# Kernel tuning notes

Hardware: AMD Instinct MI355X
Metric: run time of the kernel (lower is better)

## Reference

```python
import jax, jax.numpy as jnp
import numpy as np


def _ste_sign(x):
    # sign with straight-through (identity) gradient, matching gradient_override_map({'Sign': 'Identity'})
    return x + jax.lax.stop_gradient(jnp.sign(x) - x)


def _ternarize(W):
    # threshold = 0.7 * mean(|W|)
    t = 0.7 * jnp.mean(jnp.abs(W))
    # alpha = mean of |W| over entries with |W| strictly beyond threshold
    pos = jnp.where(W > t, W, jnp.zeros_like(W))
    neg = jnp.where(W < -t, W, jnp.zeros_like(W))
    a = jnp.abs(pos + neg)
    n = jnp.sum(jnp.where(a > 0, jnp.ones_like(a), jnp.zeros_like(a)))
    alpha = jnp.sum(a) / n
    # ternary weights in {-1, 0, +1}: sign(sign(W+t) + sign(W-t))
    Wq = _ste_sign(_ste_sign(W + t) + _ste_sign(W - t))
    return alpha * Wq


def setup_inputs() -> dict:
    key = jax.random.key(0)
    kx, kw = jax.random.split(key)
    x = jax.random.normal(kx, (32, 56, 56, 256), dtype=jnp.float32)      # NHWC
    W = jax.random.normal(kw, (3, 3, 256, 256), dtype=jnp.float32) * 0.02  # HWIO, stddev=0.02 init
    b = jnp.zeros((256,), dtype=jnp.float32)
    return {"x": x, "W": W, "b": b}


def reference(x, W, b):
    Wq = _ternarize(W)
    y = jax.lax.conv_general_dilated(
        x, Wq,
        window_strides=(1, 1),
        padding='SAME',
        dimension_numbers=('NHWC', 'HWIO', 'NHWC'),
    )
    return y + b  # act = identity
```

## Files before the change

kernel.cpp:

```cpp
#include <hip/hip_runtime.h>
#include <hip/hip_bf16.h>
#include <stdint.h>


typedef __attribute__((ext_vector_type(8))) short short8;
typedef __attribute__((ext_vector_type(4))) float floatx4;

#define Q40 1099511627776.0
#define INV_Q40 (1.0 / 1099511627776.0)
#define NW_ELEMS 589824
#define K_TOTAL 2304
#define WQT_OFF 512
#define XPAD_OFF 2360320
#define RED_BLOCKS 288

__device__ __forceinline__ void async16(const void* g, void* l) {
  __builtin_amdgcn_global_load_lds(
      (const __attribute__((address_space(1))) void*)g,
      (__attribute__((address_space(3))) void*)l, 16, 0, 0);
}

__device__ __forceinline__ ushort f2bf(float f) {
  __hip_bfloat16 h = __float2bfloat16(f);
  return *reinterpret_cast<ushort*>(&h);
}

__global__ __launch_bounds__(256) void pad_kernel(const float* __restrict__ x,
                                                  ushort* __restrict__ xpad) {
  uint idx = blockIdx.x * 256 + threadIdx.x;
  uint c8 = idx & 31;
  uint sp = idx >> 5;
  uint ww = sp % 58;
  uint t = sp / 58;
  uint hh = t % 58;
  uint n = t / 58;
  ushort* dst = xpad + ((size_t)sp * 256 + c8 * 8);
  if (hh == 0 || hh == 57 || ww == 0 || ww == 57) {
    uint4 z = {0, 0, 0, 0};
    *(uint4*)dst = z;
  } else {
    const float* src = x + (((size_t)(n * 56 + (hh - 1)) * 56 + (ww - 1)) * 256 + c8 * 8);
    float4 f0 = *(const float4*)src;
    float4 f1 = *(const float4*)(src + 4);
    ushort u[8];
    u[0] = f2bf(f0.x); u[1] = f2bf(f0.y); u[2] = f2bf(f0.z); u[3] = f2bf(f0.w);
    u[4] = f2bf(f1.x); u[5] = f2bf(f1.y); u[6] = f2bf(f1.z); u[7] = f2bf(f1.w);
    *(uint4*)dst = *(uint4*)u;
  }
}

__global__ __launch_bounds__(256) void sumabs_kernel(const float* __restrict__ W,
                                                     unsigned long long* __restrict__ scal) {
  __shared__ double sds[4];
  double v = 0.0;
#pragma unroll
  for (int j = 0; j < 8; j++) {
    uint i = (blockIdx.x * 8 + j) * 256 + threadIdx.x;
    v += (double)fabsf(W[i]);
  }
#pragma unroll
  for (int off = 32; off; off >>= 1) v += __shfl_down(v, off);
  if ((threadIdx.x & 63) == 0) sds[threadIdx.x >> 6] = v;
  __syncthreads();
  if (threadIdx.x == 0) {
    double s = sds[0] + sds[1] + sds[2] + sds[3];
    atomicAdd(&scal[0], (unsigned long long)(s * Q40 + 0.5));
  }
}

__global__ __launch_bounds__(256) void quant_kernel(const float* __restrict__ W,
                                                    ushort* __restrict__ WqT,
                                                    unsigned long long* __restrict__ scal) {
  __shared__ double sds[4];
  __shared__ unsigned long long cds[4];
  double s = (double)scal[0] * INV_Q40;
  float t = (float)(0.7 * (s / (double)NW_ELEMS));
  double v = 0.0;
  unsigned long long cnt = 0;
#pragma unroll
  for (int j = 0; j < 8; j++) {
    uint i = (blockIdx.x * 8 + j) * 256 + threadIdx.x;
    float w = W[i];
    bool pos = (w > t), neg = (w < -t);
    ushort q = pos ? (ushort)0x3F80 : (neg ? (ushort)0xBF80 : (ushort)0);
    uint k = i >> 8, co = i & 255;
    WqT[(size_t)co * K_TOTAL + k] = q;
    if (pos || neg) { v += (double)fabsf(w); cnt++; }
  }
#pragma unroll
  for (int off = 32; off; off >>= 1) {
    v += __shfl_down(v, off);
    cnt += __shfl_down(cnt, off);
  }
  if ((threadIdx.x & 63) == 0) { sds[threadIdx.x >> 6] = v; cds[threadIdx.x >> 6] = cnt; }
  __syncthreads();
  if (threadIdx.x == 0) {
    double sv = sds[0] + sds[1] + sds[2] + sds[3];
    unsigned long long sc = cds[0] + cds[1] + cds[2] + cds[3];
    atomicAdd(&scal[1], (unsigned long long)(sv * Q40 + 0.5));
    atomicAdd(&scal[2], sc);
  }
}

__global__ __launch_bounds__(256, 2) void conv_kernel(
    const ushort* __restrict__ xpad, const ushort* __restrict__ WqT,
    const unsigned long long* __restrict__ scal, const float* __restrict__ bias,
    float* __restrict__ out) {
  __shared__ __attribute__((aligned(16))) ushort Alds[128 * 64];
  __shared__ __attribute__((aligned(16))) ushort Blds[128 * 64];
  uint tid = threadIdx.x;
  uint bm = blockIdx.x >> 1, bn = blockIdx.x & 1;

  uint chunk = tid & 7;
  uint rbase = tid >> 3;
  const ushort* asrc[4];
  const ushort* bsrc[4];
#pragma unroll
  for (int i = 0; i < 4; i++) {
    uint row = i * 32 + rbase;
    uint gm = bm * 128 + row;
    uint n = gm / 3136;
    uint rem = gm - n * 3136;
    uint h = rem / 56;
    uint w = rem - h * 56;
    asrc[i] = xpad + (((size_t)(n * 58 + h) * 58 + w) * 256 + chunk * 8);
    bsrc[i] = WqT + ((size_t)(bn * 128 + row) * K_TOTAL + chunk * 8);
  }

  floatx4 acc[4][4];
#pragma unroll
  for (int mt = 0; mt < 4; mt++)
#pragma unroll
    for (int nt = 0; nt < 4; nt++) acc[mt][nt] = (floatx4){0.f, 0.f, 0.f, 0.f};

  uint lane = tid & 63;
  uint wv = tid >> 6;
  uint wm = wv >> 1, wn = wv & 1;
  uint fr = lane & 15, fq = lane >> 4;
  uint a_off = (wm * 64 + fr) * 128 + fq * 16;
  uint b_off = (wn * 64 + fr) * 128 + fq * 16;

  for (int ks = 0; ks < 36; ks++) {
    uint tap = (uint)ks >> 2;
    uint kc = ((uint)ks & 3) * 64;
    uint ky = tap / 3;
    uint kx = tap - ky * 3;
    uint aoffe = (ky * 58 + kx) * 256 + kc;
    uint boffe = (uint)ks * 64;

    __syncthreads();
#pragma unroll
    for (int i = 0; i < 4; i++)
      async16(asrc[i] + aoffe, (char*)Alds + i * 4096 + tid * 16);
#pragma unroll
    for (int i = 0; i < 4; i++)
      async16(bsrc[i] + boffe, (char*)Blds + i * 4096 + tid * 16);
    __syncthreads();

#pragma unroll
    for (int kk = 0; kk < 2; kk++) {
      short8 af[4], bfr[4];
#pragma unroll
      for (int mt = 0; mt < 4; mt++)
        af[mt] = *(const short8*)((const char*)Alds + a_off + mt * 2048 + kk * 64);
#pragma unroll
      for (int nt = 0; nt < 4; nt++)
        bfr[nt] = *(const short8*)((const char*)Blds + b_off + nt * 2048 + kk * 64);
#pragma unroll
      for (int mt = 0; mt < 4; mt++)
#pragma unroll
        for (int nt = 0; nt < 4; nt++)
          acc[mt][nt] = __builtin_amdgcn_mfma_f32_16x16x32_bf16(
              af[mt], bfr[nt], acc[mt][nt], 0, 0, 0);
    }
  }

  double sb = (double)scal[1] * INV_Q40;
  double cb = (double)scal[2];
  float alpha = (float)(sb / cb);
#pragma unroll
  for (int mt = 0; mt < 4; mt++) {
    uint mb = bm * 128 + wm * 64 + mt * 16 + fq * 4;
#pragma unroll
    for (int r = 0; r < 4; r++) {
      float* orow = out + (size_t)(mb + r) * 256;
#pragma unroll
      for (int nt = 0; nt < 4; nt++) {
        uint n = bn * 128 + wn * 64 + nt * 16 + fr;
        orow[n] = acc[mt][nt][r] * alpha + bias[n];
      }
    }
  }
}

extern "C" void kernel_launch(void* const* d_in, const int* in_sizes, int n_in,
                              void* d_out, int out_size, void* d_ws, size_t ws_size,
                              hipStream_t stream) {
  const float* x = (const float*)d_in[0];
  const float* W = (const float*)d_in[1];
  const float* b = (const float*)d_in[2];
  float* out = (float*)d_out;

  unsigned long long* scal = (unsigned long long*)d_ws;
  ushort* WqT = (ushort*)((char*)d_ws + WQT_OFF);
  ushort* xpad = (ushort*)((char*)d_ws + XPAD_OFF);

  hipMemsetAsync(d_ws, 0, 512, stream);

  pad_kernel<<<13454, 256, 0, stream>>>(x, xpad);
  sumabs_kernel<<<RED_BLOCKS, 256, 0, stream>>>(W, scal);
  quant_kernel<<<RED_BLOCKS, 256, 0, stream>>>(W, WqT, scal);
  conv_kernel<<<1568, 256, 0, stream>>>(xpad, WqT, scal, b, out);
}
```

Before: 349.4 us.

## Swizzle conv LDS tiles, reorder K loop by channel chunk, fuse pad with sumabs

```diff
diff --git a/kernel.cpp b/kernel.cpp
--- a/kernel.cpp
+++ b/kernel.cpp
@@ -13,6 +13,7 @@
 #define WQT_OFF 512
 #define XPAD_OFF 2360320
 #define RED_BLOCKS 288
+#define PAD_BLOCKS 13454
 
 __device__ __forceinline__ void async16(const void* g, void* l) {
   __builtin_amdgcn_global_load_lds(
@@ -25,9 +26,28 @@
   return *reinterpret_cast<ushort*>(&h);
 }
 
-__global__ __launch_bounds__(256) void pad_kernel(const float* __restrict__ x,
-                                                  ushort* __restrict__ xpad) {
-  uint idx = blockIdx.x * 256 + threadIdx.x;
+__global__ __launch_bounds__(256) void pad_sumabs_kernel(
+    const float* __restrict__ x, ushort* __restrict__ xpad,
+    const float* __restrict__ W, unsigned long long* __restrict__ scal) {
+  if (blockIdx.x < RED_BLOCKS) {
+    __shared__ double sds[4];
+    double v = 0.0;
+#pragma unroll
+    for (int j = 0; j < 8; j++) {
+      uint i = (blockIdx.x * 8 + j) * 256 + threadIdx.x;
+      v += (double)fabsf(W[i]);
+    }
+#pragma unroll
+    for (int off = 32; off; off >>= 1) v += __shfl_down(v, off);
+    if ((threadIdx.x & 63) == 0) sds[threadIdx.x >> 6] = v;
+    __syncthreads();
+    if (threadIdx.x == 0) {
+      double s = sds[0] + sds[1] + sds[2] + sds[3];
+      atomicAdd(&scal[0], (unsigned long long)(s * Q40 + 0.5));
+    }
+    return;
+  }
+  uint idx = (blockIdx.x - RED_BLOCKS) * 256 + threadIdx.x;
   uint c8 = idx & 31;
   uint sp = idx >> 5;
   uint ww = sp % 58;
@@ -49,25 +69,6 @@
   }
 }
 
-__global__ __launch_bounds__(256) void sumabs_kernel(const float* __restrict__ W,
-                                                     unsigned long long* __restrict__ scal) {
-  __shared__ double sds[4];
-  double v = 0.0;
-#pragma unroll
-  for (int j = 0; j < 8; j++) {
-    uint i = (blockIdx.x * 8 + j) * 256 + threadIdx.x;
-    v += (double)fabsf(W[i]);
-  }
-#pragma unroll
-  for (int off = 32; off; off >>= 1) v += __shfl_down(v, off);
-  if ((threadIdx.x & 63) == 0) sds[threadIdx.x >> 6] = v;
-  __syncthreads();
-  if (threadIdx.x == 0) {
-    double s = sds[0] + sds[1] + sds[2] + sds[3];
-    atomicAdd(&scal[0], (unsigned long long)(s * Q40 + 0.5));
-  }
-}
-
 __global__ __launch_bounds__(256) void quant_kernel(const float* __restrict__ W,
                                                     ushort* __restrict__ WqT,
                                                     unsigned long long* __restrict__ scal) {
@@ -113,6 +114,7 @@
 
   uint chunk = tid & 7;
   uint rbase = tid >> 3;
+  uint ceff = chunk ^ (rbase & 7);
   const ushort* asrc[4];
   const ushort* bsrc[4];
 #pragma unroll
@@ -123,8 +125,8 @@
     uint rem = gm - n * 3136;
     uint h = rem / 56;
     uint w = rem - h * 56;
-    asrc[i] = xpad + (((size_t)(n * 58 + h) * 58 + w) * 256 + chunk * 8);
-    bsrc[i] = WqT + ((size_t)(bn * 128 + row) * K_TOTAL + chunk * 8);
+    asrc[i] = xpad + (((size_t)(n * 58 + h) * 58 + w) * 256 + ceff * 8);
+    bsrc[i] = WqT + ((size_t)(bn * 128 + row) * K_TOTAL + ceff * 8);
   }
 
   floatx4 acc[4][4];
@@ -137,16 +139,17 @@
   uint wv = tid >> 6;
   uint wm = wv >> 1, wn = wv & 1;
   uint fr = lane & 15, fq = lane >> 4;
-  uint a_off = (wm * 64 + fr) * 128 + fq * 16;
-  uint b_off = (wn * 64 + fr) * 128 + fq * 16;
+  uint a_row = (wm * 64 + fr) * 128;
+  uint b_row = (wn * 64 + fr) * 128;
+  uint swz = (fr & 7) * 16;
 
   for (int ks = 0; ks < 36; ks++) {
-    uint tap = (uint)ks >> 2;
-    uint kc = ((uint)ks & 3) * 64;
+    uint kcq = (uint)ks / 9;
+    uint tap = (uint)ks - kcq * 9;
     uint ky = tap / 3;
     uint kx = tap - ky * 3;
-    uint aoffe = (ky * 58 + kx) * 256 + kc;
-    uint boffe = (uint)ks * 64;
+    uint aoffe = (ky * 58 + kx) * 256 + kcq * 64;
+    uint boffe = tap * 256 + kcq * 64;
 
     __syncthreads();
 #pragma unroll
@@ -159,13 +162,14 @@
 
 #pragma unroll
     for (int kk = 0; kk < 2; kk++) {
+      uint csl = ((uint)(kk * 64) + fq * 16) ^ swz;
       short8 af[4], bfr[4];
 #pragma unroll
       for (int mt = 0; mt < 4; mt++)
-        af[mt] = *(const short8*)((const char*)Alds + a_off + mt * 2048 + kk * 64);
+        af[mt] = *(const short8*)((const char*)Alds + a_row + mt * 2048 + csl);
 #pragma unroll
       for (int nt = 0; nt < 4; nt++)
-        bfr[nt] = *(const short8*)((const char*)Blds + b_off + nt * 2048 + kk * 64);
+        bfr[nt] = *(const short8*)((const char*)Blds + b_row + nt * 2048 + csl);
 #pragma unroll
       for (int mt = 0; mt < 4; mt++)
 #pragma unroll
@@ -206,9 +210,7 @@
   ushort* xpad = (ushort*)((char*)d_ws + XPAD_OFF);
 
   hipMemsetAsync(d_ws, 0, 512, stream);
-
-  pad_kernel<<<13454, 256, 0, stream>>>(x, xpad);
-  sumabs_kernel<<<RED_BLOCKS, 256, 0, stream>>>(W, scal);
+  pad_sumabs_kernel<<<RED_BLOCKS + PAD_BLOCKS, 256, 0, stream>>>(x, xpad, W, scal);
   quant_kernel<<<RED_BLOCKS, 256, 0, stream>>>(W, WqT, scal);
   conv_kernel<<<1568, 256, 0, stream>>>(xpad, WqT, scal, b, out);
 }
```

New measurement: 298.9 us. 14.5% less time.
